# Kernel optimization log

Measured on AMD Instinct MI355X. Metric: run time of the kernel, lower is better.

The kernel has to match this reference:

```python
import jax, jax.numpy as jnp
import numpy as np

EPS = 1e-15

def setup_inputs() -> dict:
    key = jax.random.key(0)
    k1, k2, k3 = jax.random.split(key, 3)
    N, DIN, DOUT = 8192, 256, 256
    x = jax.random.normal(k1, (N, DIN), dtype=jnp.float32)
    A = jax.random.uniform(k2, (N, N), dtype=jnp.float32)
    W = jax.random.normal(k3, (DOUT, DIN), dtype=jnp.float32) * (1.0 / np.sqrt(DIN))
    return {"x": x, "A": A, "W": W}

def reference(x, A, W):
    # D = sign(relu(A - eps)) -> binary edge mask; deg_i = 1 + row sum
    mask = jnp.sign(jax.nn.relu(A - EPS))
    d = (1.0 + jnp.sum(mask, axis=1)) ** (-0.5)  # [N] diagonal of D
    N = A.shape[0]
    A_tilde = A + jnp.eye(N, dtype=A.dtype)       # A + I (square case)
    h = x @ W.T                                   # [N, DOUT] linear, no bias
    # diag(d) @ A_tilde @ diag(d) as row/col scaling (same math as diag matmuls)
    A_norm = d[:, None] * A_tilde * d[None, :]
    out = jax.nn.relu(A_norm @ h)
    return (out.astype(jnp.float32), A)
```

## Files before the change

### kernel.cpp

```cpp
#include <hip/hip_runtime.h>
#include <hip/hip_bf16.h>

constexpr int NN = 8192;
constexpr int DD = 256;

typedef __bf16 bf16_t;
typedef __bf16 bf16x8 __attribute__((ext_vector_type(8)));
typedef __bf16 bf16x4 __attribute__((ext_vector_type(4)));
typedef float  floatx4 __attribute__((ext_vector_type(4)));

__global__ __launch_bounds__(256) void k1_deg_copy(const float* __restrict__ A,
                                                   float* __restrict__ Aout,
                                                   float* __restrict__ dvec) {
    const int row = blockIdx.x;
    const int t = threadIdx.x;
    const float4* __restrict__ src = (const float4*)(A + (size_t)row * NN);
    float4* __restrict__ dst = (float4*)(Aout + (size_t)row * NN);
    int cnt = 0;
#pragma unroll
    for (int i = 0; i < 8; ++i) {
        float4 v = src[t + 256 * i];
        dst[t + 256 * i] = v;
        cnt += (v.x > 1e-15f) + (v.y > 1e-15f) + (v.z > 1e-15f) + (v.w > 1e-15f);
    }
#pragma unroll
    for (int off = 32; off > 0; off >>= 1) cnt += __shfl_down(cnt, off, 64);
    __shared__ int wsum[4];
    if ((t & 63) == 0) wsum[t >> 6] = cnt;
    __syncthreads();
    if (t == 0) {
        int total = wsum[0] + wsum[1] + wsum[2] + wsum[3];
        dvec[row] = rsqrtf(1.0f + (float)total);
    }
}

__device__ inline bf16x8 load_cvt8(const float* __restrict__ p) {
    float4 v0 = *(const float4*)p;
    float4 v1 = *(const float4*)(p + 4);
    bf16x8 r;
    r[0] = (bf16_t)v0.x; r[1] = (bf16_t)v0.y; r[2] = (bf16_t)v0.z; r[3] = (bf16_t)v0.w;
    r[4] = (bf16_t)v1.x; r[5] = (bf16_t)v1.y; r[6] = (bf16_t)v1.z; r[7] = (bf16_t)v1.w;
    return r;
}

__global__ __launch_bounds__(256) void k2_h_gt(const float* __restrict__ x,
                                               const float* __restrict__ W,
                                               const float* __restrict__ dvec,
                                               bf16_t* __restrict__ gT,
                                               float* __restrict__ out) {
    const int t = threadIdx.x;
    const int l = t & 63, w = t >> 6;
    const int lm = l & 15, q = l >> 4;
    const int nb = blockIdx.x & 3, jb = blockIdx.x >> 2;
    const int n0 = nb * 64 + w * 16;
    const int j0 = jb * 128;

    floatx4 acc[8] = {};
#pragma unroll
    for (int kt = 0; kt < 256; kt += 32) {
        const int k = kt + q * 8;
        bf16x8 a = load_cvt8(W + (size_t)(n0 + lm) * DD + k);
#pragma unroll
        for (int jt = 0; jt < 8; ++jt) {
            bf16x8 b = load_cvt8(x + (size_t)(j0 + jt * 16 + lm) * DD + k);
            acc[jt] = __builtin_amdgcn_mfma_f32_16x16x32_bf16(a, b, acc[jt], 0, 0, 0);
        }
    }
#pragma unroll
    for (int jt = 0; jt < 8; ++jt) {
        const int j = j0 + jt * 16 + lm;
        const float dj = dvec[j];
#pragma unroll
        for (int r = 0; r < 4; ++r) {
            const int n = n0 + q * 4 + r;
            const float hv = acc[jt][r];
            gT[(size_t)n * NN + j] = (bf16_t)(dj * hv);
            out[(size_t)j * DD + n] = dj * dj * hv;
        }
    }
}

__global__ __launch_bounds__(256) void k3_gemm(const float* __restrict__ A,
                                               const bf16_t* __restrict__ gT,
                                               const float* __restrict__ dvec,
                                               float* __restrict__ out) {
    __shared__ __align__(16) bf16_t As[32 * 136];
    __shared__ float sd[32];
    const int t = threadIdx.x;
    const int l = t & 63, w = t >> 6;
    const int lm = l & 15, q = l >> 4;
    const int mblk = blockIdx.x & 255, ks = blockIdx.x >> 8;
    const int m0 = mblk * 32;
    const int k0 = ks * 2048;

    if (t < 32) sd[t] = dvec[m0 + t];

    floatx4 acc[2][4] = {};
    for (int kt = 0; kt < 2048; kt += 128) {
        __syncthreads();
#pragma unroll
        for (int i = 0; i < 4; ++i) {
            const int f = t + 256 * i;
            const int row = f >> 5, c4 = f & 31;
            float4 v = *(const float4*)(A + (size_t)(m0 + row) * NN + (k0 + kt) + c4 * 4);
            const float dm = sd[row];
            bf16x4 s;
            s[0] = (bf16_t)(v.x * dm); s[1] = (bf16_t)(v.y * dm);
            s[2] = (bf16_t)(v.z * dm); s[3] = (bf16_t)(v.w * dm);
            *(bf16x4*)(&As[row * 136 + c4 * 4]) = s;
        }
        __syncthreads();
#pragma unroll
        for (int kk = 0; kk < 128; kk += 32) {
            bf16x8 a0 = *(const bf16x8*)(&As[lm * 136 + kk + q * 8]);
            bf16x8 a1 = *(const bf16x8*)(&As[(16 + lm) * 136 + kk + q * 8]);
            const size_t kg = (size_t)(k0 + kt + kk + q * 8);
#pragma unroll
            for (int nt = 0; nt < 4; ++nt) {
                bf16x8 b = *(const bf16x8*)(gT + (size_t)(w * 64 + nt * 16 + lm) * NN + kg);
                acc[0][nt] = __builtin_amdgcn_mfma_f32_16x16x32_bf16(a0, b, acc[0][nt], 0, 0, 0);
                acc[1][nt] = __builtin_amdgcn_mfma_f32_16x16x32_bf16(a1, b, acc[1][nt], 0, 0, 0);
            }
        }
    }
#pragma unroll
    for (int mt = 0; mt < 2; ++mt)
#pragma unroll
        for (int nt = 0; nt < 4; ++nt)
#pragma unroll
            for (int r = 0; r < 4; ++r) {
                const int m = m0 + mt * 16 + q * 4 + r;
                const int n = w * 64 + nt * 16 + lm;
                atomicAdd(out + (size_t)m * DD + n, acc[mt][nt][r]);
            }
}

__global__ __launch_bounds__(256) void k4_relu(float* __restrict__ out) {
    const int idx = blockIdx.x * 256 + threadIdx.x;
    float4* p = (float4*)out;
    float4 v = p[idx];
    v.x = fmaxf(v.x, 0.f); v.y = fmaxf(v.y, 0.f);
    v.z = fmaxf(v.z, 0.f); v.w = fmaxf(v.w, 0.f);
    p[idx] = v;
}

extern "C" void kernel_launch(void* const* d_in, const int* in_sizes, int n_in,
                              void* d_out, int out_size, void* d_ws, size_t ws_size,
                              hipStream_t stream) {
    const float* x = (const float*)d_in[0];
    const float* A = (const float*)d_in[1];
    const float* W = (const float*)d_in[2];
    float* out0 = (float*)d_out;
    float* out1 = out0 + (size_t)NN * DD;
    float* dvec = (float*)d_ws;
    bf16_t* gT = (bf16_t*)((char*)d_ws + 32768);

    k1_deg_copy<<<NN, 256, 0, stream>>>(A, out1, dvec);
    k2_h_gt<<<256, 256, 0, stream>>>(x, W, dvec, gT, out0);
    k3_gemm<<<1024, 256, 0, stream>>>(A, gT, dvec, out0);
    k4_relu<<<(NN * DD / 4) / 256, 256, 0, stream>>>(out0);
}
```

Before: 624.9 us.

## Double-buffer A tiles via direct global-to-LDS loads in aggregation GEMM

The main A·g GEMM now stages raw fp32 A tiles straight into LDS with global_load_lds into two swizzled buffers, prefetching the next chunk while MFMAs run on the current one. The M tile grows to 64 rows with a 4x4 accumulator per wave, the split-K grows to 1024, and the row scaling by d moves from the staging step to the atomic epilogue. The goal is to hide A-load latency and raise reuse of the gT loads. Also in this change: the A copy in k1 uses nontemporal stores, and k2 runs on twice as many smaller blocks. In exchange, fp32 LDS tiles use more shared memory per block, and the bf16 conversion now happens on every LDS read.

```diff
diff --git a/kernel.cpp b/kernel.cpp
--- a/kernel.cpp
+++ b/kernel.cpp
@@ -6,21 +6,23 @@
 
 typedef __bf16 bf16_t;
 typedef __bf16 bf16x8 __attribute__((ext_vector_type(8)));
-typedef __bf16 bf16x4 __attribute__((ext_vector_type(4)));
 typedef float  floatx4 __attribute__((ext_vector_type(4)));
+
+#define GLOBAL_AS __attribute__((address_space(1)))
+#define LDS_AS    __attribute__((address_space(3)))
 
 __global__ __launch_bounds__(256) void k1_deg_copy(const float* __restrict__ A,
                                                    float* __restrict__ Aout,
                                                    float* __restrict__ dvec) {
     const int row = blockIdx.x;
     const int t = threadIdx.x;
-    const float4* __restrict__ src = (const float4*)(A + (size_t)row * NN);
-    float4* __restrict__ dst = (float4*)(Aout + (size_t)row * NN);
+    const floatx4* __restrict__ src = (const floatx4*)(A + (size_t)row * NN);
+    floatx4* __restrict__ dst = (floatx4*)(Aout + (size_t)row * NN);
     int cnt = 0;
 #pragma unroll
     for (int i = 0; i < 8; ++i) {
-        float4 v = src[t + 256 * i];
-        dst[t + 256 * i] = v;
+        floatx4 v = src[t + 256 * i];
+        __builtin_nontemporal_store(v, &dst[t + 256 * i]);
         cnt += (v.x > 1e-15f) + (v.y > 1e-15f) + (v.z > 1e-15f) + (v.w > 1e-15f);
     }
 #pragma unroll
@@ -35,8 +37,8 @@
 }
 
 __device__ inline bf16x8 load_cvt8(const float* __restrict__ p) {
-    float4 v0 = *(const float4*)p;
-    float4 v1 = *(const float4*)(p + 4);
+    floatx4 v0 = *(const floatx4*)p;
+    floatx4 v1 = *(const floatx4*)(p + 4);
     bf16x8 r;
     r[0] = (bf16_t)v0.x; r[1] = (bf16_t)v0.y; r[2] = (bf16_t)v0.z; r[3] = (bf16_t)v0.w;
     r[4] = (bf16_t)v1.x; r[5] = (bf16_t)v1.y; r[6] = (bf16_t)v1.z; r[7] = (bf16_t)v1.w;
@@ -53,21 +55,21 @@
     const int lm = l & 15, q = l >> 4;
     const int nb = blockIdx.x & 3, jb = blockIdx.x >> 2;
     const int n0 = nb * 64 + w * 16;
-    const int j0 = jb * 128;
-
-    floatx4 acc[8] = {};
+    const int j0 = jb * 64;
+
+    floatx4 acc[4] = {};
 #pragma unroll
     for (int kt = 0; kt < 256; kt += 32) {
         const int k = kt + q * 8;
         bf16x8 a = load_cvt8(W + (size_t)(n0 + lm) * DD + k);
 #pragma unroll
-        for (int jt = 0; jt < 8; ++jt) {
+        for (int jt = 0; jt < 4; ++jt) {
             bf16x8 b = load_cvt8(x + (size_t)(j0 + jt * 16 + lm) * DD + k);
             acc[jt] = __builtin_amdgcn_mfma_f32_16x16x32_bf16(a, b, acc[jt], 0, 0, 0);
         }
     }
 #pragma unroll
-    for (int jt = 0; jt < 8; ++jt) {
+    for (int jt = 0; jt < 4; ++jt) {
         const int j = j0 + jt * 16 + lm;
         const float dj = dvec[j];
 #pragma unroll
@@ -80,65 +82,101 @@
     }
 }
 
-__global__ __launch_bounds__(256) void k3_gemm(const float* __restrict__ A,
-                                               const bf16_t* __restrict__ gT,
-                                               const float* __restrict__ dvec,
-                                               float* __restrict__ out) {
-    __shared__ __align__(16) bf16_t As[32 * 136];
-    __shared__ float sd[32];
+__global__ __launch_bounds__(256, 3) void k3_gemm(const float* __restrict__ A,
+                                                  const bf16_t* __restrict__ gT,
+                                                  const float* __restrict__ dvec,
+                                                  float* __restrict__ out) {
+    __shared__ __align__(16) float As[2][64 * 64];
+    __shared__ float sd[64];
     const int t = threadIdx.x;
     const int l = t & 63, w = t >> 6;
     const int lm = l & 15, q = l >> 4;
-    const int mblk = blockIdx.x & 255, ks = blockIdx.x >> 8;
-    const int m0 = mblk * 32;
-    const int k0 = ks * 2048;
-
-    if (t < 32) sd[t] = dvec[m0 + t];
-
-    floatx4 acc[2][4] = {};
-    for (int kt = 0; kt < 2048; kt += 128) {
+    const int mblk = blockIdx.x & 127, ks = blockIdx.x >> 7;
+    const int m0 = mblk * 64;
+    const int k0 = ks * 1024;
+
+    if (t < 64) sd[t] = dvec[m0 + t];
+
+    auto stage = [&](const float* Abase, int kc, float* buf) {
+#pragma unroll
+        for (int j = 0; j < 4; ++j) {
+            const int p = j * 256 + t;
+            const int m = p >> 4;
+            const int klog = (p & 15) ^ (m & 15);
+            const float* src = Abase + (size_t)(m0 + m) * NN + kc + klog * 4;
+            float* ldsb = buf + (size_t)(j * 256 + w * 64) * 4;
+            __builtin_amdgcn_global_load_lds((const GLOBAL_AS void*)src,
+                                             (LDS_AS void*)ldsb, 16, 0, 0);
+        }
+    };
+    auto read_a = [&](const float* buf, int m, int u0) -> bf16x8 {
+        const int s = m & 15;
+        const floatx4 f0 = *(const floatx4*)(buf + (size_t)(m * 16 + (u0 ^ s)) * 4);
+        const floatx4 f1 = *(const floatx4*)(buf + (size_t)(m * 16 + ((u0 + 1) ^ s)) * 4);
+        bf16x8 r;
+        r[0] = (bf16_t)f0.x; r[1] = (bf16_t)f0.y; r[2] = (bf16_t)f0.z; r[3] = (bf16_t)f0.w;
+        r[4] = (bf16_t)f1.x; r[5] = (bf16_t)f1.y; r[6] = (bf16_t)f1.z; r[7] = (bf16_t)f1.w;
+        return r;
+    };
+
+    floatx4 acc[4][4] = {};
+    const bf16_t* gb = gT + (size_t)(w * 64 + lm) * NN + k0 + q * 8;
+
+    stage(A, k0, As[0]);
+    __syncthreads();
+    for (int c = 0; c < 16; ++c) {
+        if (c + 1 < 16) stage(A, k0 + (c + 1) * 64, As[(c + 1) & 1]);
+        const float* buf = As[c & 1];
+#pragma unroll
+        for (int kk = 0; kk < 64; kk += 32) {
+            const size_t kg = (size_t)(c * 64 + kk);
+            bf16x8 b0 = *(const bf16x8*)(gb + 0 * 16 * NN + kg);
+            bf16x8 b1 = *(const bf16x8*)(gb + 1 * 16 * NN + kg);
+            bf16x8 b2 = *(const bf16x8*)(gb + 2 * 16 * NN + kg);
+            bf16x8 b3 = *(const bf16x8*)(gb + 3 * 16 * NN + kg);
+            const int u0 = (kk >> 2) + 2 * q;
+            bf16x8 a0 = read_a(buf, 0 * 16 + lm, u0);
+            bf16x8 a1 = read_a(buf, 1 * 16 + lm, u0);
+            bf16x8 a2 = read_a(buf, 2 * 16 + lm, u0);
+            bf16x8 a3 = read_a(buf, 3 * 16 + lm, u0);
+            acc[0][0] = __builtin_amdgcn_mfma_f32_16x16x32_bf16(a0, b0, acc[0][0], 0, 0, 0);
+            acc[0][1] = __builtin_amdgcn_mfma_f32_16x16x32_bf16(a0, b1, acc[0][1], 0, 0, 0);
+            acc[0][2] = __builtin_amdgcn_mfma_f32_16x16x32_bf16(a0, b2, acc[0][2], 0, 0, 0);
+            acc[0][3] = __builtin_amdgcn_mfma_f32_16x16x32_bf16(a0, b3, acc[0][3], 0, 0, 0);
+            acc[1][0] = __builtin_amdgcn_mfma_f32_16x16x32_bf16(a1, b0, acc[1][0], 0, 0, 0);
+            acc[1][1] = __builtin_amdgcn_mfma_f32_16x16x32_bf16(a1, b1, acc[1][1], 0, 0, 0);
+            acc[1][2] = __builtin_amdgcn_mfma_f32_16x16x32_bf16(a1, b2, acc[1][2], 0, 0, 0);
+            acc[1][3] = __builtin_amdgcn_mfma_f32_16x16x32_bf16(a1, b3, acc[1][3], 0, 0, 0);
+            acc[2][0] = __builtin_amdgcn_mfma_f32_16x16x32_bf16(a2, b0, acc[2][0], 0, 0, 0);
+            acc[2][1] = __builtin_amdgcn_mfma_f32_16x16x32_bf16(a2, b1, acc[2][1], 0, 0, 0);
+            acc[2][2] = __builtin_amdgcn_mfma_f32_16x16x32_bf16(a2, b2, acc[2][2], 0, 0, 0);
+            acc[2][3] = __builtin_amdgcn_mfma_f32_16x16x32_bf16(a2, b3, acc[2][3], 0, 0, 0);
+            acc[3][0] = __builtin_amdgcn_mfma_f32_16x16x32_bf16(a3, b0, acc[3][0], 0, 0, 0);
+            acc[3][1] = __builtin_amdgcn_mfma_f32_16x16x32_bf16(a3, b1, acc[3][1], 0, 0, 0);
+            acc[3][2] = __builtin_amdgcn_mfma_f32_16x16x32_bf16(a3, b2, acc[3][2], 0, 0, 0);
+            acc[3][3] = __builtin_amdgcn_mfma_f32_16x16x32_bf16(a3, b3, acc[3][3], 0, 0, 0);
+        }
         __syncthreads();
-#pragma unroll
-        for (int i = 0; i < 4; ++i) {
-            const int f = t + 256 * i;
-            const int row = f >> 5, c4 = f & 31;
-            float4 v = *(const float4*)(A + (size_t)(m0 + row) * NN + (k0 + kt) + c4 * 4);
-            const float dm = sd[row];
-            bf16x4 s;
-            s[0] = (bf16_t)(v.x * dm); s[1] = (bf16_t)(v.y * dm);
-            s[2] = (bf16_t)(v.z * dm); s[3] = (bf16_t)(v.w * dm);
-            *(bf16x4*)(&As[row * 136 + c4 * 4]) = s;
-        }
-        __syncthreads();
-#pragma unroll
-        for (int kk = 0; kk < 128; kk += 32) {
-            bf16x8 a0 = *(const bf16x8*)(&As[lm * 136 + kk + q * 8]);
-            bf16x8 a1 = *(const bf16x8*)(&As[(16 + lm) * 136 + kk + q * 8]);
-            const size_t kg = (size_t)(k0 + kt + kk + q * 8);
+    }
+#pragma unroll
+    for (int mt = 0; mt < 4; ++mt)
+#pragma unroll
+        for (int r = 0; r < 4; ++r) {
+            const int mrow = mt * 16 + q * 4 + r;
+            const float dm = sd[mrow];
+            const int m = m0 + mrow;
 #pragma unroll
             for (int nt = 0; nt < 4; ++nt) {
-                bf16x8 b = *(const bf16x8*)(gT + (size_t)(w * 64 + nt * 16 + lm) * NN + kg);
-                acc[0][nt] = __builtin_amdgcn_mfma_f32_16x16x32_bf16(a0, b, acc[0][nt], 0, 0, 0);
-                acc[1][nt] = __builtin_amdgcn_mfma_f32_16x16x32_bf16(a1, b, acc[1][nt], 0, 0, 0);
+                const int n = w * 64 + nt * 16 + lm;
+                atomicAdd(out + (size_t)m * DD + n, dm * acc[mt][nt][r]);
             }
         }
-    }
-#pragma unroll
-    for (int mt = 0; mt < 2; ++mt)
-#pragma unroll
-        for (int nt = 0; nt < 4; ++nt)
-#pragma unroll
-            for (int r = 0; r < 4; ++r) {
-                const int m = m0 + mt * 16 + q * 4 + r;
-                const int n = w * 64 + nt * 16 + lm;
-                atomicAdd(out + (size_t)m * DD + n, acc[mt][nt][r]);
-            }
 }
 
 __global__ __launch_bounds__(256) void k4_relu(float* __restrict__ out) {
     const int idx = blockIdx.x * 256 + threadIdx.x;
-    float4* p = (float4*)out;
-    float4 v = p[idx];
+    floatx4* p = (floatx4*)out;
+    floatx4 v = p[idx];
     v.x = fmaxf(v.x, 0.f); v.y = fmaxf(v.y, 0.f);
     v.z = fmaxf(v.z, 0.f); v.w = fmaxf(v.w, 0.f);
     p[idx] = v;
@@ -156,7 +194,7 @@
     bf16_t* gT = (bf16_t*)((char*)d_ws + 32768);
 
     k1_deg_copy<<<NN, 256, 0, stream>>>(A, out1, dvec);
-    k2_h_gt<<<256, 256, 0, stream>>>(x, W, dvec, gT, out0);
+    k2_h_gt<<<512, 256, 0, stream>>>(x, W, dvec, gT, out0);
     k3_gemm<<<1024, 256, 0, stream>>>(A, gT, dvec, out0);
     k4_relu<<<(NN * DD / 4) / 256, 256, 0, stream>>>(out0);
 }
```

After: 608.6 us. 2.6% less time.
